# Optimization experiments

Hardware: AMD Instinct MI355X
Metric: run time of the kernel (lower is better)

Reference implementation:

```python
import jax, jax.numpy as jnp
import numpy as np

B, T, D, H, K = 2, 1024, 1024, 16, 64
DMIX, DDEC, DA = 32, 64, 64
EPS = 1e-5 * 64  # GroupNorm eps = 1e-5 * head_size_divisor**2


def setup_inputs() -> dict:
    keys = jax.random.split(jax.random.key(0), 12)
    r01 = 12.0 / 23.0   # layer_id / (num_hidden_layers - 1)
    r1a0 = 0.5          # 1 - layer_id / num_hidden_layers
    ddd = np.arange(D, dtype=np.float32) / D
    maa = lambda p: jnp.asarray((1.0 - ddd ** p).reshape(1, 1, D), jnp.float32)
    decay = -6.0 + 5.0 * (np.arange(D, dtype=np.float32) / (D - 1)) ** (0.7 + 1.3 * r01)
    u = lambda i, s: jax.random.uniform(keys[i], s, jnp.float32, -0.01, 0.01)
    lin = lambda i: jax.random.normal(keys[i], (D, D), jnp.float32) / np.sqrt(D)
    return dict(
        x=jax.random.normal(keys[0], (B, T, D), jnp.float32),
        time_maa_x=maa(r1a0), time_maa_w=maa(r1a0), time_maa_k=maa(r1a0),
        time_maa_v=jnp.asarray((1.0 - (ddd ** r1a0 + 0.3 * r01)).reshape(1, 1, D), jnp.float32),
        time_maa_r=maa(0.5 * r1a0), time_maa_g=maa(0.5 * r1a0), time_maa_a=maa(r1a0),
        time_maa_w1=u(1, (D, DMIX * 6)), time_maa_w2=u(2, (6, DMIX, D)),
        time_decay=jnp.asarray(decay.reshape(1, 1, D), jnp.float32),
        time_decay_w1=u(3, (D, DDEC)), time_decay_w2=u(4, (DDEC, D)),
        a0=jnp.zeros((1, 1, D), jnp.float32),
        a1=u(5, (D, DA)) * 10.0,
        a2=jax.random.normal(keys[6], (DA, D), jnp.float32) * 0.1,
        k_k=jnp.full((1, 1, D), 0.85, jnp.float32),
        k_a=jnp.ones((1, 1, D), jnp.float32),
        W_r=lin(7), W_k=lin(8), W_v=lin(9), W_g=lin(10), W_o=lin(11),
        ln_w=jnp.ones((D,), jnp.float32), ln_b=jnp.zeros((D,), jnp.float32),
    )


def reference(x, time_maa_x, time_maa_w, time_maa_k, time_maa_v, time_maa_r,
              time_maa_g, time_maa_a, time_maa_w1, time_maa_w2, time_decay,
              time_decay_w1, time_decay_w2, a0, a1, a2, k_k, k_a,
              W_r, W_k, W_v, W_g, W_o, ln_w, ln_b):
    Bx, Tx, Dx = x.shape
    # bidirectional token shift: mean of left/right neighbors
    left = jnp.pad(x[:, :-1], ((0, 0), (1, 0), (0, 0)))
    right = jnp.pad(x[:, 1:], ((0, 0), (0, 1), (0, 0)))
    dxprev = (left + right) * 0.5 - x

    # data-dependent mixing coefficients (6-way LoRA)
    xxx = x + dxprev * time_maa_x
    hmix = jnp.tanh(xxx @ time_maa_w1).reshape(Bx, Tx, 6, DMIX)
    mix = jnp.einsum('btsm,smd->sbtd', hmix, time_maa_w2)  # (6,B,T,D)
    mw, mk, mv, mr, mg, ma = mix
    xw = x + dxprev * (time_maa_w + mw)
    xk = x + dxprev * (time_maa_k + mk)
    xv = x + dxprev * (time_maa_v + mv)
    xr = x + dxprev * (time_maa_r + mr)
    xg = x + dxprev * (time_maa_g + mg)
    xa = x + dxprev * (time_maa_a + ma)

    r = xr @ W_r
    k = xk @ W_k
    v = xv @ W_v
    g = jax.nn.silu(xg @ W_g)
    w = time_decay + jnp.tanh(xw @ time_decay_w1) @ time_decay_w2
    iclr = jax.nn.sigmoid(a0 + (xa @ a1) @ a2)
    kkh = (k * k_k).reshape(Bx, Tx, H, K)
    kk = kkh / jnp.maximum(jnp.linalg.norm(kkh, axis=-1, keepdims=True), 1e-12)
    kk = kk.reshape(Bx, Tx, Dx)
    k = k * (1.0 + (iclr - 1.0) * k_a)

    heads = lambda t: t.reshape(Bx, Tx, H, K).transpose(0, 2, 1, 3)  # (B,H,T,K)
    r_h, k_h, v_h, kk_h, iclr_h = map(heads, (r, k, v, kk, iclr))
    w_h = -jnp.exp(heads(w))

    # LION bidirectional attention with delta correction (quadratic form)
    cs = jnp.cumsum(w_h, axis=2)
    cs_b = cs - w_h
    cs_f = jnp.clip(cs - cs[:, :, Tx // 2:Tx // 2 + 1, :], -60.0, 60.0)
    cs_bs = jnp.clip(cs_b - cs_b[:, :, Tx // 2:Tx // 2 + 1, :], -60.0, 60.0)
    A_fwd = jnp.tril(jnp.einsum('bhik,bhjk->bhij', r_h * jnp.exp(cs_f), k_h * jnp.exp(-cs_f)))
    A_bwd = jnp.triu(jnp.einsum('bhik,bhjk->bhij', r_h * jnp.exp(-cs_bs), k_h * jnp.exp(cs_bs)), k=1)
    kk_corr = jnp.einsum('bhik,bhjk->bhij', kk_h * iclr_h, kk_h)
    A_df = -jnp.tril(A_fwd @ jnp.tril(kk_corr, -1))
    A_db = -jnp.triu(A_bwd @ jnp.triu(kk_corr, 1), k=1)
    y = (A_fwd + A_bwd + A_df + A_db) @ v_h  # (B,H,T,K)

    # GroupNorm(n_head groups) over flattened tokens
    y = y.transpose(0, 2, 1, 3).reshape(Bx * Tx, H, K)
    mu = y.mean(axis=-1, keepdims=True)
    var = y.var(axis=-1, keepdims=True)
    y = (y - mu) / jnp.sqrt(var + EPS)
    y = y.reshape(Bx, Tx, Dx) * ln_w + ln_b
    return (y * g) @ W_o
```

## Files before the change

kernel.cpp:

```cpp
#include <hip/hip_runtime.h>
#include <math.h>

#define BB 2
#define TT 1024
#define DD 1024
#define HH 16
#define KK 64
#define NBT 2048
#define NE  2097152ULL

typedef unsigned short u16;
typedef __attribute__((ext_vector_type(8))) short short8;
typedef __attribute__((ext_vector_type(4))) short short4v;
typedef __attribute__((ext_vector_type(4))) float f32x4;

__device__ __forceinline__ float bf2f(u16 u) {
  union { unsigned int i; float f; } v; v.i = ((unsigned int)u) << 16; return v.f;
}
__device__ __forceinline__ u16 f2bf(float x) {
  union { float f; unsigned int u; } v; v.f = x;
  unsigned int r = v.u + 0x7fffu + ((v.u >> 16) & 1u);
  return (u16)(r >> 16);
}
__device__ __forceinline__ f32x4 MFMA(short8 a, short8 b, f32x4 c) {
  return __builtin_amdgcn_mfma_f32_16x16x32_bf16(a, b, c, 0, 0, 0);
}
__device__ __forceinline__ int swzb(int row, int kbyte) {
  return row * 128 + (kbyte ^ ((row & 7) << 4));
}
__device__ __forceinline__ void gload16(const void* g, void* l) {
  __builtin_amdgcn_global_load_lds((const __attribute__((address_space(1))) void*)g,
                                   (__attribute__((address_space(3))) void*)l, 16, 0, 0);
}

__global__ __launch_bounds__(256)
void pre(const float* __restrict__ W_r, const float* __restrict__ W_k,
         const float* __restrict__ W_v, const float* __restrict__ W_g,
         const float* __restrict__ W_o,
         u16* __restrict__ TR, u16* __restrict__ TK, u16* __restrict__ TV,
         u16* __restrict__ TG, u16* __restrict__ TO,
         const float* __restrict__ W2, u16* __restrict__ W2t,
         const float* __restrict__ W1, u16* __restrict__ W1t,
         const float* __restrict__ wdec2, const float* __restrict__ a2,
         u16* __restrict__ wdec2t, u16* __restrict__ a2t,
         const float* __restrict__ wdec1, const float* __restrict__ a1,
         u16* __restrict__ wdec1t, u16* __restrict__ a1t,
         const float* __restrict__ x, const float* __restrict__ maa_x,
         u16* __restrict__ xxx_b) {
  __shared__ float tl[64][65];
  int idx = blockIdx.x;
  int tid = threadIdx.x;
  if (idx < 1280) {
    int z = idx >> 8, rem = idx & 255;
    const float* W = (z == 0) ? W_r : (z == 1) ? W_k : (z == 2) ? W_v : (z == 3) ? W_g : W_o;
    u16* Wt = (z == 0) ? TR : (z == 1) ? TK : (z == 2) ? TV : (z == 3) ? TG : TO;
    int k0 = (rem & 15) * 64, n0 = (rem >> 4) * 64;
    int r = tid >> 2, c0 = (tid & 3) * 16;
#pragma unroll
    for (int j = 0; j < 16; j += 4) {
      f32x4 v = *(const f32x4*)(W + (size_t)(k0 + r) * 1024 + n0 + c0 + j);
      tl[r][c0 + j + 0] = v[0]; tl[r][c0 + j + 1] = v[1];
      tl[r][c0 + j + 2] = v[2]; tl[r][c0 + j + 3] = v[3];
    }
    __syncthreads();
    u16 o[16];
#pragma unroll
    for (int j = 0; j < 16; ++j) o[j] = f2bf(tl[c0 + j][r]);
    *(short8*)(Wt + (size_t)(n0 + r) * 1024 + k0 + c0) = *(short8*)(o);
    *(short8*)(Wt + (size_t)(n0 + r) * 1024 + k0 + c0 + 8) = *(short8*)(o + 8);
  } else if (idx < 1376) {
    int i = idx - 1280;
    int s = i >> 4, d0 = (i & 15) * 64;
    int c = tid & 63, r0 = (tid >> 6) * 8;
#pragma unroll
    for (int j = 0; j < 8; ++j)
      tl[r0 + j][c] = W2[(size_t)(s * 32 + r0 + j) * 1024 + d0 + c];
    __syncthreads();
    int d = tid >> 2, ms = (tid & 3) * 8;
    u16 o[8];
#pragma unroll
    for (int j = 0; j < 8; ++j) o[j] = f2bf(tl[ms + j][d]);
    *(short8*)(W2t + ((size_t)s * 1024 + d0 + d) * 32 + ms) = *(short8*)o;
  } else if (idx < 1424) {
    int i = idx - 1376;
    int k0 = (i & 15) * 64, n0 = (i >> 4) * 64;
    int r = tid >> 2, c0 = (tid & 3) * 16;
#pragma unroll
    for (int j = 0; j < 16; j += 4) {
      f32x4 v = *(const f32x4*)(W1 + (size_t)(k0 + r) * 192 + n0 + c0 + j);
      tl[r][c0 + j + 0] = v[0]; tl[r][c0 + j + 1] = v[1];
      tl[r][c0 + j + 2] = v[2]; tl[r][c0 + j + 3] = v[3];
    }
    __syncthreads();
    u16 o[16];
#pragma unroll
    for (int j = 0; j < 16; ++j) o[j] = f2bf(tl[c0 + j][r]);
    *(short8*)(W1t + (size_t)(n0 + r) * 1024 + k0 + c0) = *(short8*)(o);
    *(short8*)(W1t + (size_t)(n0 + r) * 1024 + k0 + c0 + 8) = *(short8*)(o + 8);
  } else if (idx < 1456) {
    int i = idx - 1424;
    int zz = i >> 4;
    const float* W = zz ? a2 : wdec2;
    u16* Wt = zz ? a2t : wdec2t;
    int n0 = (i & 15) * 64;
    int r = tid >> 2, c0 = (tid & 3) * 16;
#pragma unroll
    for (int j = 0; j < 16; j += 4) {
      f32x4 v = *(const f32x4*)(W + (size_t)r * 1024 + n0 + c0 + j);
      tl[r][c0 + j + 0] = v[0]; tl[r][c0 + j + 1] = v[1];
      tl[r][c0 + j + 2] = v[2]; tl[r][c0 + j + 3] = v[3];
    }
    __syncthreads();
    u16 o[16];
#pragma unroll
    for (int j = 0; j < 16; ++j) o[j] = f2bf(tl[c0 + j][r]);
    *(short8*)(Wt + (size_t)(n0 + r) * 64 + c0) = *(short8*)(o);
    *(short8*)(Wt + (size_t)(n0 + r) * 64 + c0 + 8) = *(short8*)(o + 8);
  } else if (idx < 1488) {
    int i = idx - 1456;
    int zz = i >> 4;
    const float* W = zz ? a1 : wdec1;
    u16* Wt = zz ? a1t : wdec1t;
    int k0 = (i & 15) * 64;
    int r = tid >> 2, c0 = (tid & 3) * 16;
#pragma unroll
    for (int j = 0; j < 16; j += 4) {
      f32x4 v = *(const f32x4*)(W + (size_t)(k0 + r) * 64 + c0 + j);
      tl[r][c0 + j + 0] = v[0]; tl[r][c0 + j + 1] = v[1];
      tl[r][c0 + j + 2] = v[2]; tl[r][c0 + j + 3] = v[3];
    }
    __syncthreads();
    u16 o[16];
#pragma unroll
    for (int j = 0; j < 16; ++j) o[j] = f2bf(tl[c0 + j][r]);
    *(short8*)(Wt + (size_t)r * 1024 + k0 + c0) = *(short8*)(o);
    *(short8*)(Wt + (size_t)r * 1024 + k0 + c0 + 8) = *(short8*)(o + 8);
  } else {
    int row = idx - 1488;
    int t = row & (TT - 1);
    int d0 = tid * 4;
    size_t g = (size_t)row * DD + d0;
    f32x4 xc = *(const f32x4*)(x + g);
    f32x4 xl = {0.f, 0.f, 0.f, 0.f}, xr = {0.f, 0.f, 0.f, 0.f};
    if (t != 0) xl = *(const f32x4*)(x + g - DD);
    if (t != TT - 1) xr = *(const f32x4*)(x + g + DD);
    f32x4 mx = *(const f32x4*)(maa_x + d0);
    u16 o[4];
#pragma unroll
    for (int j = 0; j < 4; ++j)
      o[j] = f2bf(xc[j] + (0.5f * (xl[j] + xr[j]) - xc[j]) * mx[j]);
    *(short4v*)(xxx_b + g) = *(short4v*)o;
  }
}

__global__ __launch_bounds__(256)
void hmix_g(const u16* __restrict__ xxx_b, const u16* __restrict__ W1t,
            float* __restrict__ P3) {
  __shared__ u16 As[4096];
  __shared__ u16 Bs[2048];
  int n0 = blockIdx.x * 64;
  int m0 = blockIdx.y * 128;
  int kb = blockIdx.z;
  int tid = threadIdx.x, w = tid >> 6, lane = tid & 63;
  int mq = w >> 1, nq = w & 1;
  f32x4 acc[4][2];
#pragma unroll
  for (int i = 0; i < 4; ++i)
#pragma unroll
    for (int j = 0; j < 2; ++j) acc[i][j] = {0.f, 0.f, 0.f, 0.f};
  for (int t = 0; t < 4; ++t) {
    int k0 = kb * 128 + t * 32;
#pragma unroll
    for (int c2 = 0; c2 < 2; ++c2) {
      int ch = w * 2 + c2;
      int row = ch * 16 + (lane >> 2);
      gload16(xxx_b + (size_t)(m0 + row) * 1024 + k0 + (lane & 3) * 8, As + ch * 512);
    }
    {
      int row = w * 16 + (lane >> 2);
      gload16(W1t + (size_t)(n0 + row) * 1024 + k0 + (lane & 3) * 8, Bs + w * 512);
    }
    __syncthreads();
    short8 a[4], b[2];
#pragma unroll
    for (int mf = 0; mf < 4; ++mf)
      a[mf] = *(const short8*)(As + (mq * 64 + mf * 16 + (lane & 15)) * 32 + (lane >> 4) * 8);
#pragma unroll
    for (int nf = 0; nf < 2; ++nf)
      b[nf] = *(const short8*)(Bs + (nq * 32 + nf * 16 + (lane & 15)) * 32 + (lane >> 4) * 8);
#pragma unroll
    for (int mf = 0; mf < 4; ++mf)
#pragma unroll
      for (int nf = 0; nf < 2; ++nf) acc[mf][nf] = MFMA(a[mf], b[nf], acc[mf][nf]);
    __syncthreads();
  }
#pragma unroll
  for (int mf = 0; mf < 4; ++mf) {
#pragma unroll
    for (int nf = 0; nf < 2; ++nf) {
      int mb = m0 + mq * 64 + mf * 16 + (lane >> 4) * 4;
      int n = n0 + nq * 32 + nf * 16 + (lane & 15);
#pragma unroll
      for (int r = 0; r < 4; ++r)
        P3[(size_t)kb * 393216 + (size_t)(mb + r) * 192 + n] = acc[mf][nf][r];
    }
  }
}

__global__ __launch_bounds__(256)
void skinny_g2b(const u16* __restrict__ A0, const u16* __restrict__ B0t,
                float* __restrict__ P0,
                const u16* __restrict__ A1, const u16* __restrict__ B1t,
                float* __restrict__ P1) {
  __shared__ u16 As[4096];
  __shared__ u16 Bs[2048];
  int m0 = blockIdx.x * 128;
  int kb = blockIdx.y;
  int z = blockIdx.z;
  const u16* A = z ? A1 : A0;
  const u16* Bt = z ? B1t : B0t;
  float* P = z ? P1 : P0;
  int tid = threadIdx.x, w = tid >> 6, lane = tid & 63;
  int mq = w >> 1, nq = w & 1;
  f32x4 acc[4][2];
#pragma unroll
  for (int i = 0; i < 4; ++i)
#pragma unroll
    for (int j = 0; j < 2; ++j) acc[i][j] = {0.f, 0.f, 0.f, 0.f};
  for (int t = 0; t < 4; ++t) {
    int k0 = kb * 128 + t * 32;
#pragma unroll
    for (int c2 = 0; c2 < 2; ++c2) {
      int ch = w * 2 + c2;
      int row = ch * 16 + (lane >> 2);
      gload16(A + (size_t)(m0 + row) * 1024 + k0 + (lane & 3) * 8, As + ch * 512);
    }
    {
      int row = w * 16 + (lane >> 2);
      gload16(Bt + (size_t)row * 1024 + k0 + (lane & 3) * 8, Bs + w * 512);
    }
    __syncthreads();
    short8 a[4], b[2];
#pragma unroll
    for (int mf = 0; mf < 4; ++mf)
      a[mf] = *(const short8*)(As + (mq * 64 + mf * 16 + (lane & 15)) * 32 + (lane >> 4) * 8);
#pragma unroll
    for (int nf = 0; nf < 2; ++nf)
      b[nf] = *(const short8*)(Bs + (nq * 32 + nf * 16 + (lane & 15)) * 32 + (lane >> 4) * 8);
#pragma unroll
    for (int mf = 0; mf < 4; ++mf)
#pragma unroll
      for (int nf = 0; nf < 2; ++nf) acc[mf][nf] = MFMA(a[mf], b[nf], acc[mf][nf]);
    __syncthreads();
  }
#pragma unroll
  for (int mf = 0; mf < 4; ++mf) {
#pragma unroll
    for (int nf = 0; nf < 2; ++nf) {
      int mb = m0 + mq * 64 + mf * 16 + (lane >> 4) * 4;
      int n = nq * 32 + nf * 16 + (lane & 15);
#pragma unroll
      for (int r = 0; r < 4; ++r)
        P[(size_t)kb * 131072 + (size_t)(mb + r) * 64 + n] = acc[mf][nf][r];
    }
  }
}

__global__ __launch_bounds__(256)
void reduce8b(const float* __restrict__ P, u16* __restrict__ C, int total) {
  size_t i = (size_t)blockIdx.x * 256 + threadIdx.x;
  float s = 0.f;
#pragma unroll
  for (int kb = 0; kb < 8; ++kb) s += P[(size_t)kb * total + i];
  C[i] = f2bf(tanhf(s));
}

__global__ __launch_bounds__(256)
void reduce8_pairb(const float* __restrict__ Pw, const float* __restrict__ Pa,
                   u16* __restrict__ hdec_b, u16* __restrict__ ha_b) {
  int z = blockIdx.y;
  size_t i = (size_t)blockIdx.x * 256 + threadIdx.x;
  const float* P = z ? Pa : Pw;
  float s = 0.f;
#pragma unroll
  for (int kb = 0; kb < 8; ++kb) s += P[(size_t)kb * 131072 + i];
  if (z) ha_b[i] = f2bf(s);
  else hdec_b[i] = f2bf(tanhf(s));
}

__global__ __launch_bounds__(256)
void mixg(const u16* __restrict__ hmixb, const u16* __restrict__ W2t,
          const float* __restrict__ x,
          const float* __restrict__ maa_w, const float* __restrict__ maa_k,
          const float* __restrict__ maa_v, const float* __restrict__ maa_r,
          const float* __restrict__ maa_g, const float* __restrict__ maa_a,
          u16* __restrict__ xw_b, u16* __restrict__ xa_b,
          u16* __restrict__ xk_b, u16* __restrict__ xv_b,
          u16* __restrict__ xr_b, u16* __restrict__ xg_b) {
  __shared__ u16 shm[16384];
  u16* As = shm;
  u16* Bs = shm + 4096;
  u16* mixt = shm;
  int s = blockIdx.z;
  int m0 = blockIdx.y * 128, n0 = blockIdx.x * 128;
  int tid = threadIdx.x, w = tid >> 6, lane = tid & 63;
  int mq = w >> 1, nq = w & 1;
#pragma unroll
  for (int c2 = 0; c2 < 2; ++c2) {
    int ch = w * 2 + c2;
    int row = ch * 16 + (lane >> 2);
    gload16(hmixb + (size_t)(m0 + row) * 192 + s * 32 + (lane & 3) * 8, As + ch * 512);
    gload16(W2t + ((size_t)s * 1024 + n0 + row) * 32 + (lane & 3) * 8, Bs + ch * 512);
  }
  __syncthreads();
  short8 a[4], b[4];
#pragma unroll
  for (int mf = 0; mf < 4; ++mf)
    a[mf] = *(const short8*)(As + (mq * 64 + mf * 16 + (lane & 15)) * 32 + (lane >> 4) * 8);
#pragma unroll
  for (int nf = 0; nf < 4; ++nf)
    b[nf] = *(const short8*)(Bs + (nq * 64 + nf * 16 + (lane & 15)) * 32 + (lane >> 4) * 8);
  f32x4 acc[4][4];
#pragma unroll
  for (int mf = 0; mf < 4; ++mf)
#pragma unroll
    for (int nf = 0; nf < 4; ++nf) {
      f32x4 z = {0.f, 0.f, 0.f, 0.f};
      acc[mf][nf] = MFMA(a[mf], b[nf], z);
    }
  __syncthreads();
#pragma unroll
  for (int mf = 0; mf < 4; ++mf) {
#pragma unroll
    for (int nf = 0; nf < 4; ++nf) {
      int col = nq * 64 + nf * 16 + (lane & 15);
#pragma unroll
      for (int r = 0; r < 4; ++r) {
        int row = mq * 64 + mf * 16 + (lane >> 4) * 4 + r;
        mixt[row * 128 + col] = f2bf(acc[mf][nf][r]);
      }
    }
  }
  __syncthreads();
  const float* maa = (s == 0) ? maa_w : (s == 1) ? maa_k : (s == 2) ? maa_v
                    : (s == 3) ? maa_r : (s == 4) ? maa_g : maa_a;
  u16* dst = (s == 0) ? xw_b : (s == 1) ? xk_b : (s == 2) ? xv_b
            : (s == 3) ? xr_b : (s == 4) ? xg_b : xa_b;
  int cg = tid & 15;
  int rowg = tid >> 4;
  int d0 = n0 + cg * 8;
  f32x4 ma0 = *(const f32x4*)(maa + d0);
  f32x4 ma1 = *(const f32x4*)(maa + d0 + 4);
#pragma unroll
  for (int rr = 0; rr < 8; ++rr) {
    int row = rr * 16 + rowg;
    int m = m0 + row;
    int t = m & (TT - 1);
    size_t g = (size_t)m * DD + d0;
    f32x4 xc0 = *(const f32x4*)(x + g);
    f32x4 xc1 = *(const f32x4*)(x + g + 4);
    f32x4 xl0 = {0.f, 0.f, 0.f, 0.f}, xl1 = {0.f, 0.f, 0.f, 0.f};
    f32x4 xr0 = {0.f, 0.f, 0.f, 0.f}, xr1 = {0.f, 0.f, 0.f, 0.f};
    if (t != 0) { xl0 = *(const f32x4*)(x + g - DD); xl1 = *(const f32x4*)(x + g - DD + 4); }
    if (t != TT - 1) { xr0 = *(const f32x4*)(x + g + DD); xr1 = *(const f32x4*)(x + g + DD + 4); }
    short8 mv = *(const short8*)(mixt + row * 128 + cg * 8);
    u16 o[8];
#pragma unroll
    for (int j = 0; j < 8; ++j) {
      float xcj = (j < 4) ? xc0[j & 3] : xc1[j & 3];
      float xlj = (j < 4) ? xl0[j & 3] : xl1[j & 3];
      float xrj = (j < 4) ? xr0[j & 3] : xr1[j & 3];
      float maj = (j < 4) ? ma0[j & 3] : ma1[j & 3];
      float dx = 0.5f * (xlj + xrj) - xcj;
      o[j] = f2bf(xcj + dx * (maj + bf2f((u16)mv[j])));
    }
    *(short8*)(dst + g) = *(short8*)o;
  }
}

__global__ __launch_bounds__(256)
void gemm_bf4(const u16* __restrict__ xr, const u16* __restrict__ xk,
              const u16* __restrict__ xv, const u16* __restrict__ xg,
              const u16* __restrict__ WtR, const u16* __restrict__ WtK,
              const u16* __restrict__ WtV, const u16* __restrict__ WtG,
              u16* __restrict__ rbuf, u16* __restrict__ kbuf,
              u16* __restrict__ vT, u16* __restrict__ gb) {
  __shared__ u16 As[2][4096];
  __shared__ u16 Bs[2][2048];
  int wgid = blockIdx.x;
  int xcd = wgid & 7, idx = wgid >> 3;
  int z = xcd >> 1, mhalf = xcd & 1;
  int mloc = idx & 7, nt = idx >> 3;
  int m0 = (mhalf * 8 + mloc) * 128;
  int n0 = nt * 64;
  const u16* A = (z == 0) ? xr : (z == 1) ? xk : (z == 2) ? xv : xg;
  const u16* Bt = (z == 0) ? WtR : (z == 1) ? WtK : (z == 2) ? WtV : WtG;
  int tid = threadIdx.x, w = tid >> 6, lane = tid & 63;
  int mq = w >> 1, nq = w & 1;
  int arow0 = (w * 2) * 16 + (lane >> 2);
  int arow1 = (w * 2 + 1) * 16 + (lane >> 2);
  int brow = w * 16 + (lane >> 2);
  int kc = (lane & 3) * 8;
  f32x4 acc[4][2];
#pragma unroll
  for (int i = 0; i < 4; ++i)
#pragma unroll
    for (int j = 0; j < 2; ++j) acc[i][j] = {0.f, 0.f, 0.f, 0.f};
  gload16(A + (size_t)(m0 + arow0) * 1024 + kc, As[0] + (w * 2) * 512);
  gload16(A + (size_t)(m0 + arow1) * 1024 + kc, As[0] + (w * 2 + 1) * 512);
  gload16(Bt + (size_t)(n0 + brow) * 1024 + kc, Bs[0] + w * 512);
  __syncthreads();
  for (int t = 0; t < 32; ++t) {
    int cur = t & 1;
    if (t < 31) {
      int kn = (t + 1) * 32;
      gload16(A + (size_t)(m0 + arow0) * 1024 + kn + kc, As[cur ^ 1] + (w * 2) * 512);
      gload16(A + (size_t)(m0 + arow1) * 1024 + kn + kc, As[cur ^ 1] + (w * 2 + 1) * 512);
      gload16(Bt + (size_t)(n0 + brow) * 1024 + kn + kc, Bs[cur ^ 1] + w * 512);
    }
    short8 a[4], b[2];
#pragma unroll
    for (int mf = 0; mf < 4; ++mf)
      a[mf] = *(const short8*)(As[cur] + (mq * 64 + mf * 16 + (lane & 15)) * 32 + (lane >> 4) * 8);
#pragma unroll
    for (int nf = 0; nf < 2; ++nf)
      b[nf] = *(const short8*)(Bs[cur] + (nq * 32 + nf * 16 + (lane & 15)) * 32 + (lane >> 4) * 8);
#pragma unroll
    for (int mf = 0; mf < 4; ++mf)
#pragma unroll
      for (int nf = 0; nf < 2; ++nf) acc[mf][nf] = MFMA(a[mf], b[nf], acc[mf][nf]);
    __syncthreads();
  }
#pragma unroll
  for (int mf = 0; mf < 4; ++mf) {
#pragma unroll
    for (int nf = 0; nf < 2; ++nf) {
      int mb = m0 + mq * 64 + mf * 16 + (lane >> 4) * 4;
      int n = n0 + nq * 32 + nf * 16 + (lane & 15);
      if (z == 2) {
        u16 o[4];
#pragma unroll
        for (int r = 0; r < 4; ++r) o[r] = f2bf(acc[mf][nf][r]);
        int b2 = mb >> 10, t = mb & 1023;
        *(short4v*)(vT + (((size_t)(b2 * HH + (n >> 6))) * KK + (n & 63)) * TT + t) = *(short4v*)o;
      } else if (z == 3) {
#pragma unroll
        for (int r = 0; r < 4; ++r) {
          int m = mb + r;
          float v = acc[mf][nf][r];
          gb[(size_t)m * 1024 + n] = f2bf(v / (1.f + __expf(-v)));
        }
      } else {
        u16* C = (z == 0) ? rbuf : kbuf;
#pragma unroll
        for (int r = 0; r < 4; ++r) {
          int m = mb + r;
          int b2 = m >> 10, t = m & 1023;
          C[(((size_t)(b2 * HH + (n >> 6))) * TT + t) * KK + (n & 63)] = f2bf(acc[mf][nf][r]);
        }
      }
    }
  }
}

__global__ __launch_bounds__(256)
void gemm_bfo(const u16* __restrict__ A, const u16* __restrict__ Bt,
              float* __restrict__ C) {
  __shared__ u16 As[2][4096];
  __shared__ u16 Bs[2][2048];
  int wgid = blockIdx.x;
  int xcd = wgid & 7, idx = wgid >> 3;
  int mloc = idx & 1, nt = idx >> 1;
  int m0 = (xcd * 2 + mloc) * 128;
  int n0 = nt * 64;
  int tid = threadIdx.x, w = tid >> 6, lane = tid & 63;
  int mq = w >> 1, nq = w & 1;
  int arow0 = (w * 2) * 16 + (lane >> 2);
  int arow1 = (w * 2 + 1) * 16 + (lane >> 2);
  int brow = w * 16 + (lane >> 2);
  int kc = (lane & 3) * 8;
  f32x4 acc[4][2];
// ... 69 lines not shown
    int row = rg * 16 + (lane >> 2);
    int kc = ks * 32 + (lane & 3) * 8;
    gload16(Bt + (size_t)(n0 + row) * 64 + kc, Bs + q * 512);
  }
  __syncthreads();
  f32x4 acc[4][2];
#pragma unroll
  for (int i = 0; i < 4; ++i)
#pragma unroll
    for (int j = 0; j < 2; ++j) acc[i][j] = {0.f, 0.f, 0.f, 0.f};
#pragma unroll
  for (int ks = 0; ks < 2; ++ks) {
    short8 a[4], b[2];
#pragma unroll
    for (int mf = 0; mf < 4; ++mf)
      a[mf] = *(const short8*)(As + ks * 4096 + (mq * 64 + mf * 16 + (lane & 15)) * 32 + (lane >> 4) * 8);
#pragma unroll
    for (int nf = 0; nf < 2; ++nf)
      b[nf] = *(const short8*)(Bs + ks * 2048 + (nq * 32 + nf * 16 + (lane & 15)) * 32 + (lane >> 4) * 8);
#pragma unroll
    for (int mf = 0; mf < 4; ++mf)
#pragma unroll
      for (int nf = 0; nf < 2; ++nf) acc[mf][nf] = MFMA(a[mf], b[nf], acc[mf][nf]);
  }
#pragma unroll
  for (int mf = 0; mf < 4; ++mf) {
#pragma unroll
    for (int nf = 0; nf < 2; ++nf) {
      int mb = m0 + mq * 64 + mf * 16 + (lane >> 4) * 4;
      int n = n0 + nq * 32 + nf * 16 + (lane & 15);
      float bv = bias[n];
#pragma unroll
      for (int r = 0; r < 4; ++r) {
        int m = mb + r;
        int b2 = m >> 10, t = m & 1023;
        float vv = acc[mf][nf][r] + bv;
        if (z) vv = 1.f / (1.f + expf(-vv));
        C[(((size_t)(b2 * HH + (n >> 6))) * TT + t) * KK + (n & 63)] = vv;
      }
    }
  }
}

__global__ __launch_bounds__(256)
void k4k5(u16* __restrict__ kbuf, u16* __restrict__ kkbuf, u16* __restrict__ kkibuf,
          const float* __restrict__ iclr, const float* __restrict__ k_k,
          const float* __restrict__ k_a,
          const float* __restrict__ csf, float* __restrict__ csbs,
          float* __restrict__ part) {
  int idx = blockIdx.x;
  int tid = threadIdx.x;
  if (idx < 8192) {
    int gid = idx * 4 + (tid >> 6);
    int lane = tid & 63;
    size_t base = (size_t)gid * 64 + lane;
    int h = (gid >> 10) & (HH - 1);
    int d = h * 64 + lane;
    float kv = bf2f(kbuf[base]);
    float ic = iclr[base];
    float kkh = kv * k_k[d];
    float ss = kkh * kkh;
#pragma unroll
    for (int off = 32; off > 0; off >>= 1) ss += __shfl_xor(ss, off);
    float nrm = fmaxf(sqrtf(ss), 1e-12f);
    float kkv = kkh / nrm;
    kkbuf[base] = f2bf(kkv);
    kkibuf[base] = f2bf(kkv * ic);
    kbuf[base] = f2bf(kv * (1.f + (ic - 1.f) * k_a[d]));
  } else {
    int bc = (idx - 8192) * 4 + (tid >> 6);
    int bh = bc >> 4, c = bc & 15;
    int lane = tid & 63;
    size_t base = (size_t)bh * TT * KK + (size_t)c * 64 * KK + lane;
    float p = 0.f;
    for (int i = 0; i < 64; ++i) {
      float wh = -expf(csf[base + (size_t)i * KK]);
      csbs[base + (size_t)i * KK] = wh;
      p += wh;
    }
    part[((size_t)bh * 16 + c) * 64 + lane] = p;
  }
}

__global__ __launch_bounds__(64)
void k5c_factor(const float* __restrict__ csbs, const float* __restrict__ part,
                const u16* __restrict__ rb, const u16* __restrict__ kb,
                u16* __restrict__ rfb, u16* __restrict__ rbb,
                u16* __restrict__ kfb, u16* __restrict__ kbw) {
  int bc = blockIdx.x;
  int bh = bc >> 4, c = bc & 15;
  int lane = threadIdx.x;
  size_t hb = (size_t)bh * TT * KK;
  float run = 0.f, csb512 = 0.f;
  for (int cc = 0; cc < 16; ++cc) {
    float pv = part[((size_t)bh * 16 + cc) * 64 + lane];
    if (cc < c) run += pv;
    if (cc < 8) csb512 += pv;
  }
  float wh512 = csbs[hb + (size_t)512 * KK + lane];
  float cs512 = csb512 + wh512;
  size_t base = hb + (size_t)c * 64 * KK + lane;
  float cs = run;
  for (int i = 0; i < 64; ++i) {
    size_t g = base + (size_t)i * KK;
    float wh = csbs[g];
    cs += wh;
    float cf = fminf(fmaxf(cs - cs512, -60.f), 60.f);
    float cb = fminf(fmaxf((cs - wh) - csb512, -60.f), 60.f);
    float rvf = bf2f(rb[g]);
    float kvf = bf2f(kb[g]);
    rfb[g] = f2bf(rvf * __expf(cf));
    kfb[g] = f2bf(kvf * __expf(-cf));
    rbb[g] = f2bf(rvf * __expf(-cb));
    kbw[g] = f2bf(kvf * __expf(cb));
  }
}

struct SReg { short8 a0, a1, b0, b1; };
template <int RSA, int RSB>
__device__ __forceinline__ void sload(const u16* ka, const u16* vb, SReg& r) {
  int t0 = threadIdx.x, t1 = threadIdx.x + 256;
  r.a0 = *(const short8*)(ka + (size_t)(t0 >> 3) * RSA + (t0 & 7) * 8);
  r.a1 = *(const short8*)(ka + (size_t)(t1 >> 3) * RSA + (t1 & 7) * 8);
  r.b0 = *(const short8*)(vb + (size_t)(t0 >> 3) * RSB + (t0 & 7) * 8);
  r.b1 = *(const short8*)(vb + (size_t)(t1 >> 3) * RSB + (t1 & 7) * 8);
}
__device__ __forceinline__ void swrite(u16* Kt, u16* Vt, const SReg& r) {
  int t0 = threadIdx.x, t1 = threadIdx.x + 256;
  *(short8*)((char*)Kt + swzb(t0 >> 3, (t0 & 7) * 16)) = r.a0;
  *(short8*)((char*)Kt + swzb(t1 >> 3, (t1 & 7) * 16)) = r.a1;
  *(short8*)((char*)Vt + swzb(t0 >> 3, (t0 & 7) * 16)) = r.b0;
  *(short8*)((char*)Vt + swzb(t1 >> 3, (t1 & 7) * 16)) = r.b1;
}
template <int MASK>
__device__ __forceinline__ void store_S(const f32x4 s[4], u16* St, int lane, int w) {
  int ig0 = w * 16 + (lane >> 4) * 4;
#pragma unroll
  for (int jf = 0; jf < 4; ++jf) {
    int jl = jf * 16 + (lane & 15);
#pragma unroll
    for (int r = 0; r < 4; ++r) {
      int il = ig0 + r;
      float v = s[jf][r];
      if (MASK == 1 && !(jl < il)) v = 0.f;
      if (MASK == 2 && !(jl > il)) v = 0.f;
      if (MASK == 3 && !(jl <= il)) v = 0.f;
      *(u16*)((char*)St + swzb(il, jl * 2)) = f2bf(v);
    }
  }
}
__device__ __forceinline__ void smm(short8 a0, short8 a1, const u16* Kt, f32x4 s[4], int lane) {
  __builtin_amdgcn_s_setprio(1);
#pragma unroll
  for (int jf = 0; jf < 4; ++jf) {
    f32x4 z = {0.f, 0.f, 0.f, 0.f};
    short8 kb0 = *(const short8*)((const char*)Kt + swzb(jf * 16 + (lane & 15), (lane >> 4) * 16));
    z = MFMA(a0, kb0, z);
    short8 kb1 = *(const short8*)((const char*)Kt + swzb(jf * 16 + (lane & 15), 64 + (lane >> 4) * 16));
    z = MFMA(a1, kb1, z);
    s[jf] = z;
  }
  __builtin_amdgcn_s_setprio(0);
}
__device__ __forceinline__ void pv(const u16* St, const u16* Vt, f32x4 acc[4], int lane, int w) {
  __builtin_amdgcn_s_setprio(1);
#pragma unroll
  for (int ks = 0; ks < 2; ++ks) {
    short8 a = *(const short8*)((const char*)St + swzb(w * 16 + (lane & 15), ks * 64 + (lane >> 4) * 16));
#pragma unroll
    for (int cf = 0; cf < 4; ++cf) {
      short8 b = *(const short8*)((const char*)Vt + swzb(cf * 16 + (lane & 15), ks * 64 + (lane >> 4) * 16));
      acc[cf] = MFMA(a, b, acc[cf]);
    }
  }
  __builtin_amdgcn_s_setprio(0);
}

__global__ __launch_bounds__(256)
void k6_pass1(const u16* __restrict__ kk, const u16* __restrict__ kki,
              const u16* __restrict__ vT, u16* __restrict__ vfT, u16* __restrict__ vbT) {
  __shared__ u16 Kt[2][4096], Vt[2][4096], St[4096];
  int wg = blockIdx.x;
  int bh = wg & 31, it = wg >> 5, i0 = it * 64;
  size_t hb = (size_t)bh * 65536;
  int tid = threadIdx.x, w = tid >> 6, lane = tid & 63;
  int iw = i0 + w * 16;
  int row = iw + (lane & 15), ko = (lane >> 4) * 8;
  short8 a0 = *(const short8*)(kki + hb + (size_t)row * 64 + ko);
  short8 a1 = *(const short8*)(kki + hb + (size_t)row * 64 + 32 + ko);
  f32x4 af[4], ab[4];
#pragma unroll
  for (int c = 0; c < 4; ++c) { af[c] = {0.f, 0.f, 0.f, 0.f}; ab[c] = {0.f, 0.f, 0.f, 0.f}; }
  SReg sr, nx;
  sload<64, 1024>(kk + hb, vT + hb, sr);
  swrite(Kt[0], Vt[0], sr);
  __syncthreads();
  for (int s = 0; s < 16; ++s) {
    int cur = s & 1;
    if (s < 15)
      sload<64, 1024>(kk + hb + (size_t)(s + 1) * 4096, vT + hb + (s + 1) * 64, nx);
    f32x4 sv[4];
    smm(a0, a1, Kt[cur], sv, lane);
    if (s == it) {
      store_S<1>(sv, St, lane, w);
      pv(St, Vt[cur], af, lane, w);
      store_S<2>(sv, St, lane, w);
      pv(St, Vt[cur], ab, lane, w);
    } else if (s < it) {
      store_S<0>(sv, St, lane, w);
      pv(St, Vt[cur], af, lane, w);
    } else {
      store_S<0>(sv, St, lane, w);
      pv(St, Vt[cur], ab, lane, w);
    }
    if (s < 15) swrite(Kt[cur ^ 1], Vt[cur ^ 1], nx);
    __syncthreads();
  }
#pragma unroll
  for (int cf = 0; cf < 4; ++cf) {
    int c = cf * 16 + (lane & 15);
    int i = iw + (lane >> 4) * 4;
    size_t g = hb + (size_t)c * 1024 + i;
    short4v vv = *(const short4v*)(vT + g);
    u16 o1[4], o2[4];
#pragma unroll
    for (int r = 0; r < 4; ++r) {
      float v0 = bf2f((u16)vv[r]);
      o1[r] = f2bf(v0 - af[cf][r]);
      o2[r] = f2bf(v0 - ab[cf][r]);
    }
    *(short4v*)(vfT + g) = *(short4v*)o1;
    *(short4v*)(vbT + g) = *(short4v*)o2;
  }
}

__global__ __launch_bounds__(256)
void k7_pass2(const u16* __restrict__ rfb, const u16* __restrict__ rbb,
              const u16* __restrict__ kfb, const u16* __restrict__ kbw,
              const u16* __restrict__ vfT, const u16* __restrict__ vbT,
              float* __restrict__ y) {
  __shared__ u16 Kt[2][4096], Vt[2][4096], St[4096];
  int wg = blockIdx.x;
  int bh = wg & 31, it = wg >> 5, i0 = it * 64;
  size_t hb = (size_t)bh * 65536;
  int tid = threadIdx.x, w = tid >> 6, lane = tid & 63;
  int iw = i0 + w * 16;
  int row = iw + (lane & 15), ko = (lane >> 4) * 8;
  short8 rf0 = *(const short8*)(rfb + hb + (size_t)row * 64 + ko);
  short8 rf1 = *(const short8*)(rfb + hb + (size_t)row * 64 + 32 + ko);
  short8 rb0 = *(const short8*)(rbb + hb + (size_t)row * 64 + ko);
  short8 rb1 = *(const short8*)(rbb + hb + (size_t)row * 64 + 32 + ko);
  f32x4 acc[4];
#pragma unroll
  for (int c = 0; c < 4; ++c) acc[c] = {0.f, 0.f, 0.f, 0.f};
  SReg sr, nx;
  {
    sload<64, 1024>(kfb + hb, vfT + hb, sr);
    swrite(Kt[0], Vt[0], sr);
  }
  __syncthreads();
  for (int s = 0; s < 17; ++s) {
    int cur = s & 1;
    if (s < 16) {
      int s1 = s + 1;
      bool f1 = (s1 <= it);
      int j1 = f1 ? s1 : s1 - 1;
      const u16* kp = (f1 ? kfb : kbw) + hb + (size_t)j1 * 4096;
      const u16* vp = (f1 ? vfT : vbT) + hb + j1 * 64;
// ... 49 lines not shown
    float o = xn * lnw[d] + lnb[d];
    outb[(size_t)bt * DD + d] = f2bf(o * bf2f(g[(size_t)bt * DD + d]));
  }
}

extern "C" void kernel_launch(void* const* d_in, const int* in_sizes, int n_in,
                              void* d_out, int out_size, void* d_ws, size_t ws_size,
                              hipStream_t stream) {
  const float* x      = (const float*)d_in[0];
  const float* maa_x  = (const float*)d_in[1];
  const float* maa_w  = (const float*)d_in[2];
  const float* maa_k  = (const float*)d_in[3];
  const float* maa_v  = (const float*)d_in[4];
  const float* maa_r  = (const float*)d_in[5];
  const float* maa_g  = (const float*)d_in[6];
  const float* maa_a  = (const float*)d_in[7];
  const float* w1mix  = (const float*)d_in[8];
  const float* w2mix  = (const float*)d_in[9];
  const float* tdecay = (const float*)d_in[10];
  const float* wdec1  = (const float*)d_in[11];
  const float* wdec2  = (const float*)d_in[12];
  const float* a0     = (const float*)d_in[13];
  const float* a1     = (const float*)d_in[14];
  const float* a2     = (const float*)d_in[15];
  const float* k_k    = (const float*)d_in[16];
  const float* k_a    = (const float*)d_in[17];
  const float* W_r    = (const float*)d_in[18];
  const float* W_k    = (const float*)d_in[19];
  const float* W_v    = (const float*)d_in[20];
  const float* W_g    = (const float*)d_in[21];
  const float* W_o    = (const float*)d_in[22];
  const float* lnw    = (const float*)d_in[23];
  const float* lnb    = (const float*)d_in[24];
  float* out = (float*)d_out;

  const size_t NEf = NE;
  float* F = (float*)d_ws;
  u16*   xxx_b  = (u16*)F;
  float* ybuf   = F;
  u16*   xw_b   = (u16*)(F + 1 * NEf);
  u16*   xa_b   = (u16*)(F + 2 * NEf);
  float* csfb   = F + 3 * NEf;
  float* csbsb  = F + 4 * NEf;
  float* P3     = F + 3 * NEf;
  float* PpartW = F + 3 * NEf;
  float* PpartA = F + 4 * NEf;
  float* iclr   = F + 5 * NEf;
  u16*   gb     = (u16*)(F + 6 * NEf);
  u16*   hmixb  = (u16*)(F + 7 * NEf);
  u16*   hdec_b = (u16*)(F + 7 * NEf + 524288);
  u16*   ha_b   = (u16*)(F + 7 * NEf + 786432);
  float* partb  = F + 7 * NEf + 917504;
  u16*   W1t    = (u16*)(F + 7 * NEf + 1048576);
  u16*   wdec2t = (u16*)(F + 7 * NEf + 1146880);
  u16*   a2t    = (u16*)(F + 7 * NEf + 1179648);
  u16*   wdec1t = (u16*)(F + 7 * NEf + 1212416);
  u16*   a1t    = (u16*)(F + 7 * NEf + 1245184);
  u16*   W2t    = (u16*)(F + 7 * NEf + 1966080);
  u16* rfb = (u16*)xw_b;
  u16* rbb = rfb + NEf;
  u16* kfb = (u16*)xa_b;
  u16* kbw = kfb + NEf;
  u16* U = (u16*)(F + 8 * NEf);
  u16* xr_b = U + 0 * NEf;
  u16* xk_b = U + 1 * NEf;
  u16* xv_b = U + 2 * NEf;
  u16* xg_b = U + 3 * NEf;
  u16* rbuf = U + 4 * NEf;
  u16* kbuf = U + 5 * NEf;
  u16* vT   = U + 6 * NEf;
  u16* kkb  = U + 7 * NEf;
  u16* kkib = U + 8 * NEf;
  u16* vfT  = U + 9 * NEf;
  u16* vbT  = U + 10 * NEf;
  u16* gnb  = U + 11 * NEf;
  u16* WtR  = U + 12 * NEf;
  u16* WtK  = U + 12 * NEf + 1048576;
  u16* WtV  = U + 12 * NEf + 2097152;
  u16* WtG  = U + 12 * NEf + 3145728;
  u16* WtO  = U + 12 * NEf + 4194304;

  dim3 blk(256);

  pre<<<3536, blk, 0, stream>>>(W_r, W_k, W_v, W_g, W_o, WtR, WtK, WtV, WtG, WtO,
                                w2mix, W2t, w1mix, W1t, wdec2, a2, wdec2t, a2t,
                                wdec1, a1, wdec1t, a1t,
                                x, maa_x, xxx_b);

  hmix_g<<<dim3(3, 16, 8), blk, 0, stream>>>(xxx_b, W1t, P3);
  reduce8b<<<1536, blk, 0, stream>>>(P3, hmixb, 393216);

  mixg<<<dim3(8, 16, 6), blk, 0, stream>>>(hmixb, W2t, x,
                                           maa_w, maa_k, maa_v, maa_r, maa_g, maa_a,
                                           xw_b, xa_b, xk_b, xv_b, xr_b, xg_b);

  skinny_g2b<<<dim3(16, 8, 2), blk, 0, stream>>>(xw_b, wdec1t, PpartW,
                                                 xa_b, a1t, PpartA);
  reduce8_pairb<<<dim3(512, 2), blk, 0, stream>>>(PpartW, PpartA, hdec_b, ha_b);
  gemm_k2b<<<dim3(16, 16, 2), blk, 0, stream>>>(hdec_b, wdec2t, csfb, tdecay,
                                                ha_b, a2t, iclr, a0);

  gemm_bf4<<<1024, blk, 0, stream>>>(xr_b, xk_b, xv_b, xg_b,
                                     WtR, WtK, WtV, WtG,
                                     rbuf, kbuf, vT, gb);

  k4k5<<<8320, blk, 0, stream>>>(kbuf, kkb, kkib, iclr, k_k, k_a,
                                 csfb, csbsb, partb);
  k5c_factor<<<512, 64, 0, stream>>>(csbsb, partb, rbuf, kbuf, rfb, rbb, kfb, kbw);
  k6_pass1<<<512, blk, 0, stream>>>(kkb, kkib, vT, vfT, vbT);
  k7_pass2<<<512, blk, 0, stream>>>(rfb, rbb, kfb, kbw, vfT, vbT, ybuf);
  k8_gnorm<<<NBT, blk, 0, stream>>>(ybuf, gb, lnw, lnb, gnb);
  gemm_bfo<<<256, blk, 0, stream>>>(gnb, WtO, out);
}
```

Baseline: 193.1 us.

## Merge independent kernels into shared launches to overlap work and cut launches

Moves the large weight-transpose blocks from the pre kernel into the hmix_g launch. Folds the skinny decay/a LoRA GEMM into gemm_bf4 as extra blocks, and folds k5c_factor into k6_pass1 as extra blocks with four 64-lane groups per block. Each pair of independent workloads now shares one grid, which removes launches and lets small or tail-heavy kernels fill idle CUs. The cost is extra shared memory in hmix_g, which may lower occupancy, and heterogeneous block mixes that complicate scheduling.

```diff
diff --git a/kernel.cpp b/kernel.cpp
--- a/kernel.cpp
+++ b/kernel.cpp
@@ -34,12 +34,7 @@
 }
 
 __global__ __launch_bounds__(256)
-void pre(const float* __restrict__ W_r, const float* __restrict__ W_k,
-         const float* __restrict__ W_v, const float* __restrict__ W_g,
-         const float* __restrict__ W_o,
-         u16* __restrict__ TR, u16* __restrict__ TK, u16* __restrict__ TV,
-         u16* __restrict__ TG, u16* __restrict__ TO,
-         const float* __restrict__ W2, u16* __restrict__ W2t,
+void pre(const float* __restrict__ W2, u16* __restrict__ W2t,
          const float* __restrict__ W1, u16* __restrict__ W1t,
          const float* __restrict__ wdec2, const float* __restrict__ a2,
          u16* __restrict__ wdec2t, u16* __restrict__ a2t,
@@ -50,27 +45,8 @@
   __shared__ float tl[64][65];
   int idx = blockIdx.x;
   int tid = threadIdx.x;
-  if (idx < 1280) {
-    int z = idx >> 8, rem = idx & 255;
-    const float* W = (z == 0) ? W_r : (z == 1) ? W_k : (z == 2) ? W_v : (z == 3) ? W_g : W_o;
-    u16* Wt = (z == 0) ? TR : (z == 1) ? TK : (z == 2) ? TV : (z == 3) ? TG : TO;
-    int k0 = (rem & 15) * 64, n0 = (rem >> 4) * 64;
-    int r = tid >> 2, c0 = (tid & 3) * 16;
-#pragma unroll
-    for (int j = 0; j < 16; j += 4) {
-      f32x4 v = *(const f32x4*)(W + (size_t)(k0 + r) * 1024 + n0 + c0 + j);
-      tl[r][c0 + j + 0] = v[0]; tl[r][c0 + j + 1] = v[1];
-      tl[r][c0 + j + 2] = v[2]; tl[r][c0 + j + 3] = v[3];
-    }
-    __syncthreads();
-    u16 o[16];
-#pragma unroll
-    for (int j = 0; j < 16; ++j) o[j] = f2bf(tl[c0 + j][r]);
-    *(short8*)(Wt + (size_t)(n0 + r) * 1024 + k0 + c0) = *(short8*)(o);
-    *(short8*)(Wt + (size_t)(n0 + r) * 1024 + k0 + c0 + 8) = *(short8*)(o + 8);
-  } else if (idx < 1376) {
-    int i = idx - 1280;
-    int s = i >> 4, d0 = (i & 15) * 64;
+  if (idx < 96) {
+    int s = idx >> 4, d0 = (idx & 15) * 64;
     int c = tid & 63, r0 = (tid >> 6) * 8;
 #pragma unroll
     for (int j = 0; j < 8; ++j)
@@ -81,8 +57,8 @@
 #pragma unroll
     for (int j = 0; j < 8; ++j) o[j] = f2bf(tl[ms + j][d]);
     *(short8*)(W2t + ((size_t)s * 1024 + d0 + d) * 32 + ms) = *(short8*)o;
-  } else if (idx < 1424) {
-    int i = idx - 1376;
+  } else if (idx < 144) {
+    int i = idx - 96;
     int k0 = (i & 15) * 64, n0 = (i >> 4) * 64;
     int r = tid >> 2, c0 = (tid & 3) * 16;
 #pragma unroll
@@ -97,8 +73,8 @@
     for (int j = 0; j < 16; ++j) o[j] = f2bf(tl[c0 + j][r]);
     *(short8*)(W1t + (size_t)(n0 + r) * 1024 + k0 + c0) = *(short8*)(o);
     *(short8*)(W1t + (size_t)(n0 + r) * 1024 + k0 + c0 + 8) = *(short8*)(o + 8);
-  } else if (idx < 1456) {
-    int i = idx - 1424;
+  } else if (idx < 176) {
+    int i = idx - 144;
     int zz = i >> 4;
     const float* W = zz ? a2 : wdec2;
     u16* Wt = zz ? a2t : wdec2t;
@@ -116,8 +92,8 @@
     for (int j = 0; j < 16; ++j) o[j] = f2bf(tl[c0 + j][r]);
     *(short8*)(Wt + (size_t)(n0 + r) * 64 + c0) = *(short8*)(o);
     *(short8*)(Wt + (size_t)(n0 + r) * 64 + c0 + 8) = *(short8*)(o + 8);
-  } else if (idx < 1488) {
-    int i = idx - 1456;
+  } else if (idx < 208) {
+    int i = idx - 176;
     int zz = i >> 4;
     const float* W = zz ? a1 : wdec1;
     u16* Wt = zz ? a1t : wdec1t;
@@ -136,7 +112,7 @@
     *(short8*)(Wt + (size_t)r * 1024 + k0 + c0) = *(short8*)(o);
     *(short8*)(Wt + (size_t)r * 1024 + k0 + c0 + 8) = *(short8*)(o + 8);
   } else {
-    int row = idx - 1488;
+    int row = idx - 208;
     int t = row & (TT - 1);
     int d0 = tid * 4;
     size_t g = (size_t)row * DD + d0;
@@ -154,20 +130,50 @@
 }
 
 __global__ __launch_bounds__(256)
-void hmix_g(const u16* __restrict__ xxx_b, const u16* __restrict__ W1t,
+void hmix_g(const float* __restrict__ W_r, const float* __restrict__ W_k,
+            const float* __restrict__ W_v, const float* __restrict__ W_g,
+            const float* __restrict__ W_o,
+            u16* __restrict__ TR, u16* __restrict__ TK, u16* __restrict__ TV,
+            u16* __restrict__ TG, u16* __restrict__ TO,
+            const u16* __restrict__ xxx_b, const u16* __restrict__ W1t,
             float* __restrict__ P3) {
+  __shared__ float tl[64][65];
   __shared__ u16 As[4096];
   __shared__ u16 Bs[2048];
-  int n0 = blockIdx.x * 64;
-  int m0 = blockIdx.y * 128;
-  int kb = blockIdx.z;
-  int tid = threadIdx.x, w = tid >> 6, lane = tid & 63;
+  int idx = blockIdx.x;
+  int tid = threadIdx.x;
+  if (idx < 1280) {
+    int z = idx >> 8, rem = idx & 255;
+    const float* W = (z == 0) ? W_r : (z == 1) ? W_k : (z == 2) ? W_v : (z == 3) ? W_g : W_o;
+    u16* Wt = (z == 0) ? TR : (z == 1) ? TK : (z == 2) ? TV : (z == 3) ? TG : TO;
+    int k0 = (rem & 15) * 64, n0 = (rem >> 4) * 64;
+    int r = tid >> 2, c0 = (tid & 3) * 16;
+#pragma unroll
+    for (int j = 0; j < 16; j += 4) {
+      f32x4 v = *(const f32x4*)(W + (size_t)(k0 + r) * 1024 + n0 + c0 + j);
+      tl[r][c0 + j + 0] = v[0]; tl[r][c0 + j + 1] = v[1];
+      tl[r][c0 + j + 2] = v[2]; tl[r][c0 + j + 3] = v[3];
+    }
+    __syncthreads();
+    u16 o[16];
+#pragma unroll
+    for (int j = 0; j < 16; ++j) o[j] = f2bf(tl[c0 + j][r]);
+    *(short8*)(Wt + (size_t)(n0 + r) * 1024 + k0 + c0) = *(short8*)(o);
+    *(short8*)(Wt + (size_t)(n0 + r) * 1024 + k0 + c0 + 8) = *(short8*)(o + 8);
+    return;
+  }
+  int i = idx - 1280;
+  int n0 = (i % 3) * 64;
+  int q = i / 3;
+  int m0 = (q & 15) * 128;
+  int kb = q >> 4;
+  int w = tid >> 6, lane = tid & 63;
   int mq = w >> 1, nq = w & 1;
   f32x4 acc[4][2];
 #pragma unroll
-  for (int i = 0; i < 4; ++i)
-#pragma unroll
-    for (int j = 0; j < 2; ++j) acc[i][j] = {0.f, 0.f, 0.f, 0.f};
+  for (int ii = 0; ii < 4; ++ii)
+#pragma unroll
+    for (int j = 0; j < 2; ++j) acc[ii][j] = {0.f, 0.f, 0.f, 0.f};
   for (int t = 0; t < 4; ++t) {
     int k0 = kb * 128 + t * 32;
 #pragma unroll
@@ -203,65 +209,6 @@
 #pragma unroll
       for (int r = 0; r < 4; ++r)
         P3[(size_t)kb * 393216 + (size_t)(mb + r) * 192 + n] = acc[mf][nf][r];
-    }
-  }
-}
-
-__global__ __launch_bounds__(256)
-void skinny_g2b(const u16* __restrict__ A0, const u16* __restrict__ B0t,
-                float* __restrict__ P0,
-                const u16* __restrict__ A1, const u16* __restrict__ B1t,
-                float* __restrict__ P1) {
-  __shared__ u16 As[4096];
-  __shared__ u16 Bs[2048];
-  int m0 = blockIdx.x * 128;
-  int kb = blockIdx.y;
-  int z = blockIdx.z;
-  const u16* A = z ? A1 : A0;
-  const u16* Bt = z ? B1t : B0t;
-  float* P = z ? P1 : P0;
-  int tid = threadIdx.x, w = tid >> 6, lane = tid & 63;
-  int mq = w >> 1, nq = w & 1;
-  f32x4 acc[4][2];
-#pragma unroll
-  for (int i = 0; i < 4; ++i)
-#pragma unroll
-    for (int j = 0; j < 2; ++j) acc[i][j] = {0.f, 0.f, 0.f, 0.f};
-  for (int t = 0; t < 4; ++t) {
-    int k0 = kb * 128 + t * 32;
-#pragma unroll
-    for (int c2 = 0; c2 < 2; ++c2) {
-      int ch = w * 2 + c2;
-      int row = ch * 16 + (lane >> 2);
-      gload16(A + (size_t)(m0 + row) * 1024 + k0 + (lane & 3) * 8, As + ch * 512);
-    }
-    {
-      int row = w * 16 + (lane >> 2);
-      gload16(Bt + (size_t)row * 1024 + k0 + (lane & 3) * 8, Bs + w * 512);
-    }
-    __syncthreads();
-    short8 a[4], b[2];
-#pragma unroll
-    for (int mf = 0; mf < 4; ++mf)
-      a[mf] = *(const short8*)(As + (mq * 64 + mf * 16 + (lane & 15)) * 32 + (lane >> 4) * 8);
-#pragma unroll
-    for (int nf = 0; nf < 2; ++nf)
-      b[nf] = *(const short8*)(Bs + (nq * 32 + nf * 16 + (lane & 15)) * 32 + (lane >> 4) * 8);
-#pragma unroll
-    for (int mf = 0; mf < 4; ++mf)
-#pragma unroll
-      for (int nf = 0; nf < 2; ++nf) acc[mf][nf] = MFMA(a[mf], b[nf], acc[mf][nf]);
-    __syncthreads();
-  }
-#pragma unroll
-  for (int mf = 0; mf < 4; ++mf) {
-#pragma unroll
-    for (int nf = 0; nf < 2; ++nf) {
-      int mb = m0 + mq * 64 + mf * 16 + (lane >> 4) * 4;
-      int n = nq * 32 + nf * 16 + (lane & 15);
-#pragma unroll
-      for (int r = 0; r < 4; ++r)
-        P[(size_t)kb * 131072 + (size_t)(mb + r) * 64 + n] = acc[mf][nf][r];
     }
   }
 }
@@ -384,10 +331,68 @@
               const u16* __restrict__ WtR, const u16* __restrict__ WtK,
               const u16* __restrict__ WtV, const u16* __restrict__ WtG,
               u16* __restrict__ rbuf, u16* __restrict__ kbuf,
-              u16* __restrict__ vT, u16* __restrict__ gb) {
+              u16* __restrict__ vT, u16* __restrict__ gb,
+              const u16* __restrict__ xw_b, const u16* __restrict__ wdec1t,
+              float* __restrict__ PpartW,
+              const u16* __restrict__ xa_b, const u16* __restrict__ a1t,
+              float* __restrict__ PpartA) {
   __shared__ u16 As[2][4096];
   __shared__ u16 Bs[2][2048];
   int wgid = blockIdx.x;
+  int tid = threadIdx.x, w = tid >> 6, lane = tid & 63;
+  int mq = w >> 1, nq = w & 1;
+  if (wgid >= 1024) {
+    int i = wgid - 1024;
+    int m0 = (i & 15) * 128;
+    int kb = (i >> 4) & 7;
+    int z = i >> 7;
+    const u16* A = z ? xa_b : xw_b;
+    const u16* Bt = z ? a1t : wdec1t;
+    float* P = z ? PpartA : PpartW;
+    f32x4 acc[4][2];
+#pragma unroll
+    for (int ii = 0; ii < 4; ++ii)
+#pragma unroll
+      for (int j = 0; j < 2; ++j) acc[ii][j] = {0.f, 0.f, 0.f, 0.f};
+    for (int t = 0; t < 4; ++t) {
+      int k0 = kb * 128 + t * 32;
+#pragma unroll
+      for (int c2 = 0; c2 < 2; ++c2) {
+        int ch = w * 2 + c2;
+        int row = ch * 16 + (lane >> 2);
+        gload16(A + (size_t)(m0 + row) * 1024 + k0 + (lane & 3) * 8, As[0] + ch * 512);
+      }
+      {
+        int row = w * 16 + (lane >> 2);
+        gload16(Bt + (size_t)row * 1024 + k0 + (lane & 3) * 8, Bs[0] + w * 512);
+      }
+      __syncthreads();
+      short8 a[4], b[2];
+#pragma unroll
+      for (int mf = 0; mf < 4; ++mf)
+        a[mf] = *(const short8*)(As[0] + (mq * 64 + mf * 16 + (lane & 15)) * 32 + (lane >> 4) * 8);
+#pragma unroll
+      for (int nf = 0; nf < 2; ++nf)
+        b[nf] = *(const short8*)(Bs[0] + (nq * 32 + nf * 16 + (lane & 15)) * 32 + (lane >> 4) * 8);
+#pragma unroll
+      for (int mf = 0; mf < 4; ++mf)
+#pragma unroll
+        for (int nf = 0; nf < 2; ++nf) acc[mf][nf] = MFMA(a[mf], b[nf], acc[mf][nf]);
+      __syncthreads();
+    }
+#pragma unroll
+    for (int mf = 0; mf < 4; ++mf) {
+#pragma unroll
+      for (int nf = 0; nf < 2; ++nf) {
+        int mb = m0 + mq * 64 + mf * 16 + (lane >> 4) * 4;
+        int n = nq * 32 + nf * 16 + (lane & 15);
+#pragma unroll
+        for (int r = 0; r < 4; ++r)
+          P[(size_t)kb * 131072 + (size_t)(mb + r) * 64 + n] = acc[mf][nf][r];
+      }
+    }
+    return;
+  }
   int xcd = wgid & 7, idx = wgid >> 3;
   int z = xcd >> 1, mhalf = xcd & 1;
   int mloc = idx & 7, nt = idx >> 3;
@@ -395,8 +400,6 @@
   int n0 = nt * 64;
   const u16* A = (z == 0) ? xr : (z == 1) ? xk : (z == 2) ? xv : xg;
   const u16* Bt = (z == 0) ? WtR : (z == 1) ? WtK : (z == 2) ? WtV : WtG;
-  int tid = threadIdx.x, w = tid >> 6, lane = tid & 63;
-  int mq = w >> 1, nq = w & 1;
   int arow0 = (w * 2) * 16 + (lane >> 2);
   int arow1 = (w * 2 + 1) * 16 + (lane >> 2);
   int brow = w * 16 + (lane >> 2);
@@ -632,40 +635,6 @@
   }
 }
 
-__global__ __launch_bounds__(64)
-void k5c_factor(const float* __restrict__ csbs, const float* __restrict__ part,
-                const u16* __restrict__ rb, const u16* __restrict__ kb,
-                u16* __restrict__ rfb, u16* __restrict__ rbb,
-                u16* __restrict__ kfb, u16* __restrict__ kbw) {
-  int bc = blockIdx.x;
-  int bh = bc >> 4, c = bc & 15;
-  int lane = threadIdx.x;
-  size_t hb = (size_t)bh * TT * KK;
-  float run = 0.f, csb512 = 0.f;
-  for (int cc = 0; cc < 16; ++cc) {
-    float pv = part[((size_t)bh * 16 + cc) * 64 + lane];
-    if (cc < c) run += pv;
-    if (cc < 8) csb512 += pv;
-  }
-  float wh512 = csbs[hb + (size_t)512 * KK + lane];
-  float cs512 = csb512 + wh512;
-  size_t base = hb + (size_t)c * 64 * KK + lane;
-  float cs = run;
-  for (int i = 0; i < 64; ++i) {
-    size_t g = base + (size_t)i * KK;
-    float wh = csbs[g];
-    cs += wh;
-    float cf = fminf(fmaxf(cs - cs512, -60.f), 60.f);
-    float cb = fminf(fmaxf((cs - wh) - csb512, -60.f), 60.f);
-    float rvf = bf2f(rb[g]);
-    float kvf = bf2f(kb[g]);
-    rfb[g] = f2bf(rvf * __expf(cf));
-    kfb[g] = f2bf(kvf * __expf(-cf));
-    rbb[g] = f2bf(rvf * __expf(-cb));
-    kbw[g] = f2bf(kvf * __expf(cb));
-  }
-}
-
 struct SReg { short8 a0, a1, b0, b1; };
 template <int RSA, int RSB>
 __device__ __forceinline__ void sload(const u16* ka, const u16* vb, SReg& r) {
@@ -728,12 +697,47 @@
 
 __global__ __launch_bounds__(256)
 void k6_pass1(const u16* __restrict__ kk, const u16* __restrict__ kki,
-              const u16* __restrict__ vT, u16* __restrict__ vfT, u16* __restrict__ vbT) {
+              const u16* __restrict__ vT, u16* __restrict__ vfT, u16* __restrict__ vbT,
+              const float* __restrict__ csbs, const float* __restrict__ part,
+              const u16* __restrict__ rb, const u16* __restrict__ kb,
+              u16* __restrict__ rfb, u16* __restrict__ rbb,
+              u16* __restrict__ kfb, u16* __restrict__ kbw) {
   __shared__ u16 Kt[2][4096], Vt[2][4096], St[4096];
   int wg = blockIdx.x;
+  int tid = threadIdx.x;
+  if (wg >= 512) {
+    int bc = (wg - 512) * 4 + (tid >> 6);
+    int bh = bc >> 4, c = bc & 15;
+    int lane = tid & 63;
+    size_t hb = (size_t)bh * TT * KK;
+    float run = 0.f, csb512 = 0.f;
+    for (int cc = 0; cc < 16; ++cc) {
+      float pvv = part[((size_t)bh * 16 + cc) * 64 + lane];
+      if (cc < c) run += pvv;
+      if (cc < 8) csb512 += pvv;
+    }
+    float wh512 = csbs[hb + (size_t)512 * KK + lane];
+    float cs512 = csb512 + wh512;
+    size_t base = hb + (size_t)c * 64 * KK + lane;
+    float cs = run;
+    for (int i = 0; i < 64; ++i) {
+      size_t g = base + (size_t)i * KK;
+      float wh = csbs[g];
+      cs += wh;
+      float cf = fminf(fmaxf(cs - cs512, -60.f), 60.f);
+      float cb = fminf(fmaxf((cs - wh) - csb512, -60.f), 60.f);
+      float rvf = bf2f(rb[g]);
+      float kvf = bf2f(kb[g]);
+      rfb[g] = f2bf(rvf * __expf(cf));
+      kfb[g] = f2bf(kvf * __expf(-cf));
+      rbb[g] = f2bf(rvf * __expf(-cb));
+      kbw[g] = f2bf(kvf * __expf(cb));
+    }
+    return;
+  }
   int bh = wg & 31, it = wg >> 5, i0 = it * 64;
   size_t hb = (size_t)bh * 65536;
-  int tid = threadIdx.x, w = tid >> 6, lane = tid & 63;
+  int w = tid >> 6, lane = tid & 63;
   int iw = i0 + w * 16;
   int row = iw + (lane & 15), ko = (lane >> 4) * 8;
   short8 a0 = *(const short8*)(kki + hb + (size_t)row * 64 + ko);
@@ -949,32 +953,33 @@
 
   dim3 blk(256);
 
-  pre<<<3536, blk, 0, stream>>>(W_r, W_k, W_v, W_g, W_o, WtR, WtK, WtV, WtG, WtO,
-                                w2mix, W2t, w1mix, W1t, wdec2, a2, wdec2t, a2t,
-                                wdec1, a1, wdec1t, a1t,
-                                x, maa_x, xxx_b);
-
-  hmix_g<<<dim3(3, 16, 8), blk, 0, stream>>>(xxx_b, W1t, P3);
+  pre<<<2256, blk, 0, stream>>>(w2mix, W2t, w1mix, W1t, wdec2, a2, wdec2t, a2t,
+                                wdec1, a1, wdec1t, a1t, x, maa_x, xxx_b);
+
+  hmix_g<<<1664, blk, 0, stream>>>(W_r, W_k, W_v, W_g, W_o,
+                                   WtR, WtK, WtV, WtG, WtO,
+                                   xxx_b, W1t, P3);
   reduce8b<<<1536, blk, 0, stream>>>(P3, hmixb, 393216);
 
   mixg<<<dim3(8, 16, 6), blk, 0, stream>>>(hmixb, W2t, x,
                                            maa_w, maa_k, maa_v, maa_r, maa_g, maa_a,
                                            xw_b, xa_b, xk_b, xv_b, xr_b, xg_b);
 
-  skinny_g2b<<<dim3(16, 8, 2), blk, 0, stream>>>(xw_b, wdec1t, PpartW,
-                                                 xa_b, a1t, PpartA);
+  gemm_bf4<<<1280, blk, 0, stream>>>(xr_b, xk_b, xv_b, xg_b,
+                                     WtR, WtK, WtV, WtG,
+                                     rbuf, kbuf, vT, gb,
+                                     xw_b, wdec1t, PpartW, xa_b, a1t, PpartA);
+
   reduce8_pairb<<<dim3(512, 2), blk, 0, stream>>>(PpartW, PpartA, hdec_b, ha_b);
   gemm_k2b<<<dim3(16, 16, 2), blk, 0, stream>>>(hdec_b, wdec2t, csfb, tdecay,
                                                 ha_b, a2t, iclr, a0);
 
-  gemm_bf4<<<1024, blk, 0, stream>>>(xr_b, xk_b, xv_b, xg_b,
-                                     WtR, WtK, WtV, WtG,
-                                     rbuf, kbuf, vT, gb);
-
   k4k5<<<8320, blk, 0, stream>>>(kbuf, kkb, kkib, iclr, k_k, k_a,
                                  csfb, csbsb, partb);
-  k5c_factor<<<512, 64, 0, stream>>>(csbsb, partb, rbuf, kbuf, rfb, rbb, kfb, kbw);
-  k6_pass1<<<512, blk, 0, stream>>>(kkb, kkib, vT, vfT, vbT);
+
+  k6_pass1<<<640, blk, 0, stream>>>(kkb, kkib, vT, vfT, vbT,
+                                    csbsb, partb, rbuf, kbuf,
+                                    rfb, rbb, kfb, kbw);
   k7_pass2<<<512, blk, 0, stream>>>(rfb, rbb, kfb, kbw, vfT, vbT, ybuf);
   k8_gnorm<<<NBT, blk, 0, stream>>>(ybuf, gb, lnw, lnb, gnb);
   gemm_bfo<<<256, blk, 0, stream>>>(gnb, WtO, out);
```

Result: faster. 184.6 us (median of 2 runs) (-4.4%).
